# Performance work log

Hardware: AMD Instinct MI355X
Metric: run time of the kernel (lower is better)

Reference implementation:

```python
import jax, jax.numpy as jnp
import numpy as np

B, N, DIN, D, H, L, DOUT = 32, 512, 256, 256, 8, 2, 256
DH = D // H
EPS = 1e-5
MAX_DEG, NUM_SPATIAL = 1000, 100


def _bn(x, g, b):
    # torch BatchNorm1d training-mode normalization (biased variance over dim 0)
    m = x.mean(0)
    v = x.var(0)
    return (x - m) * jax.lax.rsqrt(v + EPS) * g + b


def _ln(x, g, b):
    m = x.mean(-1, keepdims=True)
    v = x.var(-1, keepdims=True)
    return (x - m) * jax.lax.rsqrt(v + EPS) * g + b


def _leaky(x):
    return jnp.where(x >= 0, x, 0.01 * x)


def setup_inputs() -> dict:
    key = jax.random.key(0)
    ks = iter(jax.random.split(key, 40))
    nrm = lambda shape: jax.random.normal(next(ks), shape, jnp.float32) * 0.02
    inp = {
        "x": jax.random.normal(next(ks), (B * N, DIN), jnp.float32),
        "adj_fc": jax.random.randint(next(ks), (B, N, N), 0, 2, jnp.int32),
        "spd_dist": jax.random.randint(next(ks), (B, N, N), -1, NUM_SPATIAL, jnp.int32),
        # lin_first: Linear + BatchNorm1d + LeakyReLU
        "W_first": nrm((D, DIN)), "b_first": jnp.zeros((D,), jnp.float32),
        "bn1_g": jnp.ones((D,), jnp.float32), "bn1_b": jnp.zeros((D,), jnp.float32),
        # embeddings (spd_embedding has padding_idx=0 -> zero row)
        "deg_emb": nrm((MAX_DEG, D)),
        "spd_emb": nrm((NUM_SPATIAL, H)).at[0].set(0.0),
        # stacked TransformerEncoderLayer params [L, ...]
        "Wqkv": nrm((L, 3 * D, D)), "bqkv": jnp.zeros((L, 3 * D), jnp.float32),
        "Wo": nrm((L, D, D)), "bo": jnp.zeros((L, D), jnp.float32),
        "ln1_g": jnp.ones((L, D), jnp.float32), "ln1_b": jnp.zeros((L, D), jnp.float32),
        "W1": nrm((L, D, D)), "b1": jnp.zeros((L, D), jnp.float32),
        "W2": nrm((L, D, D)), "b2": jnp.zeros((L, D), jnp.float32),
        "ln2_g": jnp.ones((L, D), jnp.float32), "ln2_b": jnp.zeros((L, D), jnp.float32),
        # lin_in: Linear + BatchNorm1d + LeakyReLU
        "W_in": nrm((DOUT, D)), "b_in": jnp.zeros((DOUT,), jnp.float32),
        "bn2_g": jnp.ones((DOUT,), jnp.float32), "bn2_b": jnp.zeros((DOUT,), jnp.float32),
    }
    return inp


def _forward(x, adj_fc, spd_dist, W_first, b_first, bn1_g, bn1_b, deg_emb, spd_emb,
             Wqkv, bqkv, Wo, bo, ln1_g, ln1_b, W1, b1, W2, b2, ln2_g, ln2_b,
             W_in, b_in, bn2_g, bn2_b):
    h = _leaky(_bn(x @ W_first.T + b_first, bn1_g, bn1_b)).reshape(B, N, D)
    # degree bias: adj_fc.bool().sum(1) -> [B, N]
    deg = (adj_fc != 0).sum(1)
    h = h + deg_emb[deg]
    # SPD-based per-head additive attention bias
    neg = spd_dist < 0
    am = spd_emb[jnp.where(neg, 0, spd_dist)]            # [B, N, N, H]
    am = jnp.where(neg[..., None], -1.0, am)
    # torch.cat over dim 0 per head -> [H*B, N, N]; torch MHA then consumes it
    # row-major as (b*H + h); replicate that exact (buggy-but-faithful) layout
    bias = jnp.concatenate([am[..., i] for i in range(H)], axis=0).reshape(B, H, N, N)
    scale = 1.0 / np.sqrt(DH).astype(np.float32)
    for l in range(L):
        qkv = h @ Wqkv[l].T + bqkv[l]                    # [B, N, 3D]
        q, k, v = jnp.split(qkv, 3, axis=-1)
        q = q.reshape(B, N, H, DH).transpose(0, 2, 1, 3)
        k = k.reshape(B, N, H, DH).transpose(0, 2, 1, 3)
        v = v.reshape(B, N, H, DH).transpose(0, 2, 1, 3)
        s = jnp.einsum('bhqd,bhkd->bhqk', q, k) * scale + bias
        p = jax.nn.softmax(s, axis=-1)
        o = jnp.einsum('bhqk,bhkd->bhqd', p, v).transpose(0, 2, 1, 3).reshape(B, N, D)
        h = _ln(h + o @ Wo[l].T + bo[l], ln1_g[l], ln1_b[l])  # post-norm
        f = jax.nn.relu(h @ W1[l].T + b1[l]) @ W2[l].T + b2[l]
        h = _ln(h + f, ln2_g[l], ln2_b[l])
    return _leaky(_bn(h.reshape(B * N, D) @ W_in.T + b_in, bn2_g, bn2_b))


def reference(x, adj_fc, spd_dist, W_first, b_first, bn1_g, bn1_b, deg_emb, spd_emb,
              Wqkv, bqkv, Wo, bo, ln1_g, ln1_b, W1, b1, W2, b2, ln2_g, ln2_b,
              W_in, b_in, bn2_g, bn2_b):
    return _forward(x, adj_fc, spd_dist, W_first, b_first, bn1_g, bn1_b, deg_emb,
                    spd_emb, Wqkv, bqkv, Wo, bo, ln1_g, ln1_b, W1, b1, W2, b2,
                    ln2_g, ln2_b, W_in, b_in, bn2_g, bn2_b)
```

## Files before the change

### kernel.cpp

```cpp
#include <hip/hip_runtime.h>
#include <hip/hip_bf16.h>
#include <math.h>

#define B_   32
#define N_   512
#define D_   256
#define H_   8
#define DH_  32
#define L_   2
#define ROWS (B_ * N_)
#define EPS_ 1e-5f

typedef __attribute__((ext_vector_type(8))) short bf16x8;
typedef __attribute__((ext_vector_type(4))) float f32x4;

__device__ __forceinline__ short f2bf(float f) {
    unsigned u = __builtin_bit_cast(unsigned, f);
    u += 0x7fffu + ((u >> 16) & 1u);
    return (short)(u >> 16);
}

__device__ __forceinline__ void gl_lds16(const short* g, short* l) {
    __builtin_amdgcn_global_load_lds(
        (const __attribute__((address_space(1))) unsigned int*)g,
        (__attribute__((address_space(3))) unsigned int*)l, 16, 0, 0);
}

__global__ __launch_bounds__(256) void cvt_all(const float* __restrict__ x,
                                               const float* __restrict__ wf,
                                               const float* __restrict__ wq,
                                               const float* __restrict__ wo,
                                               const float* __restrict__ w1,
                                               const float* __restrict__ w2,
                                               const float* __restrict__ wi,
                                               short* __restrict__ xb,
                                               short* __restrict__ wb)
{
    const int u = blockIdx.x * 256 + threadIdx.x;
    if (u >= 638976) return;
    const float* s; short* d; int off;
    if      (u < 524288) { s = x;  d = xb;          off = u; }
    else if (u < 532480) { s = wf; d = wb;          off = u - 524288; }
    else if (u < 581632) { s = wq; d = wb + 65536;  off = u - 532480; }
    else if (u < 598016) { s = wo; d = wb + 458752; off = u - 581632; }
    else if (u < 614400) { s = w1; d = wb + 589824; off = u - 598016; }
    else if (u < 630784) { s = w2; d = wb + 720896; off = u - 614400; }
    else                 { s = wi; d = wb + 851968; off = u - 630784; }
    const float4 a = ((const float4*)s)[off * 2];
    const float4 b = ((const float4*)s)[off * 2 + 1];
    bf16x8 o;
    o[0] = f2bf(a.x); o[1] = f2bf(a.y); o[2] = f2bf(a.z); o[3] = f2bf(a.w);
    o[4] = f2bf(b.x); o[5] = f2bf(b.y); o[6] = f2bf(b.z); o[7] = f2bf(b.w);
    *(bf16x8*)(d + (size_t)off * 8) = o;
}

#define GSTAGE(buf, kb)                                                        \
    {                                                                          \
        _Pragma("unroll")                                                      \
        for (int j = 0; j < 4; j++) {                                          \
            const int ra = srow + j * 8;                                       \
            const int sw = (sslot ^ (ra & 7)) << 3;                            \
            gl_lds16(A  + (size_t)(m0 + ra) * K + (kb) + sw,                   \
                     &Al[buf][(w * 32 + j * 8) * 64]);                         \
            gl_lds16(Bw + (size_t)(n0 + ra) * K + (kb) + sw,                   \
                     &Bl[buf][(w * 32 + j * 8) * 64]);                         \
        }                                                                      \
    }

template<int FLAGS>
__global__ __launch_bounds__(256) void gemm_bf16(const short* __restrict__ A,
                                                 const short* __restrict__ Bw,
                                                 const float* __restrict__ bias,
                                                 float* __restrict__ Cf,
                                                 short* __restrict__ Cb,
                                                 int M, int Nn, int K)
{
    __shared__ short Al[2][128 * 64];
    __shared__ short Bl[2][128 * 64];
    const int t = threadIdx.x, w = t >> 6, l = t & 63;
    const int lg = l >> 4, lr = l & 15;
    const int wm = w >> 1, wn = w & 1;
    const int m0 = blockIdx.x * 128, n0 = blockIdx.y * 128;
    const int srow = w * 32 + (l >> 3), sslot = l & 7;

    f32x4 acc[4][4] = {};

    GSTAGE(0, 0);
    __syncthreads();
    int cur = 0;
    for (int kb = 64; kb < K + 64; kb += 64) {
        if (kb < K) GSTAGE(cur ^ 1, kb);
        #pragma unroll
        for (int ks = 0; ks < 2; ks++) {
            bf16x8 af[4], bfr[4];
            #pragma unroll
            for (int i = 0; i < 4; i++) {
                const int ar = wm * 64 + i * 16 + lr;
                af[i]  = *(const bf16x8*)&Al[cur][ar * 64 + (((lg + ks * 4) ^ (ar & 7)) << 3)];
                const int br = wn * 64 + i * 16 + lr;
                bfr[i] = *(const bf16x8*)&Bl[cur][br * 64 + (((lg + ks * 4) ^ (br & 7)) << 3)];
            }
            #pragma unroll
            for (int mi = 0; mi < 4; mi++)
                #pragma unroll
                for (int ni = 0; ni < 4; ni++)
                    acc[mi][ni] = __builtin_amdgcn_mfma_f32_16x16x32_bf16(af[mi], bfr[ni],
                                                                          acc[mi][ni], 0, 0, 0);
        }
        __syncthreads();
        cur ^= 1;
    }

    #pragma unroll
    for (int ni = 0; ni < 4; ni++) {
        const int n = n0 + wn * 64 + ni * 16 + lr;
        const float bv = bias[n];
        const float qs = ((FLAGS & 8) && n < 256) ? 0.17677669529663687f : 1.0f;
        #pragma unroll
        for (int mi = 0; mi < 4; mi++) {
            #pragma unroll
            for (int r = 0; r < 4; r++) {
                const int m = m0 + wm * 64 + mi * 16 + 4 * lg + r;
                float v = (acc[mi][ni][r] + bv) * qs;
                if (FLAGS & 4) v = fmaxf(v, 0.f);
                if (FLAGS & 1) Cf[(size_t)m * Nn + n] = v;
                if (FLAGS & 2) Cb[(size_t)m * Nn + n] = f2bf(v);
            }
        }
    }
}

__global__ __launch_bounds__(256) void bn_partial(const float* __restrict__ Y,
                                                  float* __restrict__ part)
{
    const int t = threadIdx.x, blk = blockIdx.x;
    float s = 0.f, sq = 0.f;
    const float* p = Y + (size_t)blk * 256 * 256 + t;
    for (int r = 0; r < 256; r++) {
        float v = p[(size_t)r * 256];
        s += v; sq += v * v;
    }
    part[t * 64 + blk]         = s;
    part[16384 + t * 64 + blk] = sq;
}

__global__ __launch_bounds__(256) void bn_finalize(const float* __restrict__ part,
                                                   const float* __restrict__ g,
                                                   const float* __restrict__ b,
                                                   float* __restrict__ sc)
{
    const int t = threadIdx.x;
    float s = 0.f, sq = 0.f;
    #pragma unroll
    for (int i = 0; i < 16; i++) {
        const float4 a = *(const float4*)&part[t * 64 + i * 4];
        const float4 q = *(const float4*)&part[16384 + t * 64 + i * 4];
        s  += (a.x + a.y) + (a.z + a.w);
        sq += (q.x + q.y) + (q.z + q.w);
    }
    const float mean = s * (1.f / (float)ROWS);
    const float var  = sq * (1.f / (float)ROWS) - mean * mean;
    const float k    = g[t] * rsqrtf(var + EPS_);
    sc[t]       = k;
    sc[256 + t] = b[t] - mean * k;
}

__global__ __launch_bounds__(256) void bn_apply_leaky(const float* __restrict__ Y,
                                                      const float* __restrict__ sc,
                                                      float* __restrict__ O)
{
    const int idx = blockIdx.x * 256 + threadIdx.x;
    const int c4  = (idx & 63) * 4;
    const float4 v  = *(const float4*)&Y[(size_t)idx * 4];
    const float4 k  = *(const float4*)&sc[c4];
    const float4 sh = *(const float4*)&sc[256 + c4];
    float4 o;
    o.x = fmaf(v.x, k.x, sh.x); o.x = o.x >= 0.f ? o.x : 0.01f * o.x;
    o.y = fmaf(v.y, k.y, sh.y); o.y = o.y >= 0.f ? o.y : 0.01f * o.y;
    o.z = fmaf(v.z, k.z, sh.z); o.z = o.z >= 0.f ? o.z : 0.01f * o.z;
    o.w = fmaf(v.w, k.w, sh.w); o.w = o.w >= 0.f ? o.w : 0.01f * o.w;
    *(float4*)&O[(size_t)idx * 4] = o;
}

__global__ __launch_bounds__(256) void bn_deg(const float* __restrict__ Y,
                                              const float* __restrict__ sc,
                                              const int* __restrict__ deg,
                                              const float* __restrict__ emb,
                                              float* __restrict__ h,
                                              short* __restrict__ hb)
{
    const int idx = blockIdx.x * 256 + threadIdx.x;
    const int row = idx >> 6;
    const int c4  = (idx & 63) * 4;
    const float4 v  = *(const float4*)&Y[(size_t)idx * 4];
    const float4 k  = *(const float4*)&sc[c4];
    const float4 sh = *(const float4*)&sc[256 + c4];
    const int d = deg[row];
    const float4 e = *(const float4*)&emb[(size_t)d * 256 + c4];
    float4 o;
    o.x = fmaf(v.x, k.x, sh.x); o.x = (o.x >= 0.f ? o.x : 0.01f * o.x) + e.x;
    o.y = fmaf(v.y, k.y, sh.y); o.y = (o.y >= 0.f ? o.y : 0.01f * o.y) + e.y;
    o.z = fmaf(v.z, k.z, sh.z); o.z = (o.z >= 0.f ? o.z : 0.01f * o.z) + e.z;
    o.w = fmaf(v.w, k.w, sh.w); o.w = (o.w >= 0.f ? o.w : 0.01f * o.w) + e.w;
    *(float4*)&h[(size_t)idx * 4] = o;
    short4 s4; s4.x = f2bf(o.x); s4.y = f2bf(o.y); s4.z = f2bf(o.z); s4.w = f2bf(o.w);
    *(short4*)&hb[(size_t)idx * 4] = s4;
}

__global__ __launch_bounds__(256) void deg_kernel(const int* __restrict__ adj,
                                                  int* __restrict__ deg)
{
    __shared__ int sm[4][64];
    const int b = blockIdx.x, j0 = blockIdx.y * 64;
    const int tg = threadIdx.x >> 6, lane = threadIdx.x & 63;
    const int* p = adj + (size_t)b * N_ * N_ + j0 + lane;
    int c = 0;
    #pragma unroll 4
    for (int i = tg; i < N_; i += 4) c += (p[(size_t)i * N_] != 0);
    sm[tg][lane] = c;
    __syncthreads();
    if (threadIdx.x < 64)
        deg[b * N_ + j0 + threadIdx.x] =
            sm[0][threadIdx.x] + sm[1][threadIdx.x] + sm[2][threadIdx.x] + sm[3][threadIdx.x];
}

__global__ __launch_bounds__(256) void add_ln2(float* __restrict__ h,
                                               short* __restrict__ hb,
                                               const float* __restrict__ p,
                                               const float* __restrict__ g,
                                               const float* __restrict__ be)
{
    const int wv = threadIdx.x >> 6, ln = threadIdx.x & 63;
    const size_t row  = (size_t)blockIdx.x * 4 + wv;
    const size_t base = row * 256 + ln * 4;
    const float4 a = *(const float4*)&h[base];
    const float4 q = *(const float4*)&p[base];
    const float v0 = a.x + q.x, v1 = a.y + q.y, v2 = a.z + q.z, v3 = a.w + q.w;
    float s  = v0 + v1 + v2 + v3;
    float sq = v0 * v0 + v1 * v1 + v2 * v2 + v3 * v3;
    #pragma unroll
    for (int m = 1; m < 64; m <<= 1) {
        s  += __shfl_xor(s,  m, 64);
        sq += __shfl_xor(sq, m, 64);
    }
    const float mean = s * (1.f / 256.f);
    const float var  = sq * (1.f / 256.f) - mean * mean;
    const float r    = rsqrtf(var + EPS_);
    const float4 gg = *(const float4*)&g[ln * 4];
    const float4 bb = *(const float4*)&be[ln * 4];
    float4 o;
    o.x = (v0 - mean) * r * gg.x + bb.x;
    o.y = (v1 - mean) * r * gg.y + bb.y;
    o.z = (v2 - mean) * r * gg.z + bb.z;
    o.w = (v3 - mean) * r * gg.w + bb.w;
    *(float4*)&h[base] = o;
    short4 sb; sb.x = f2bf(o.x); sb.y = f2bf(o.y); sb.z = f2bf(o.z); sb.w = f2bf(o.w);
    *(short4*)&hb[base] = sb;
}

#define KST 40
#define VST 136
#define PST 136

__global__ __launch_bounds__(256) void attn_mfma(const short* __restrict__ qkv,
                                                 const int* __restrict__ spd,
                                                 const float* __restrict__ semb,
                                                 short* __restrict__ out)
{
    __shared__ short Kl[128 * KST];
    __shared__ short Vl[32 * VST + 64];
    __shared__ short Pl[4][16 * PST];
    __shared__ float sembL[128];

    const int t  = threadIdx.x, w = t >> 6, l = t & 63;
    const int lg = l >> 4, lr = l & 15;

    const int s   = ((blockIdx.x & 7) << 7) + (blockIdx.x >> 3);
    const int bs  = s >> 5, ie = (s >> 2) & 7, qb = s & 3;
    const int b   = (ie * 32 + bs) >> 3, hd = (ie * 32 + bs) & 7;
    const int q0  = qb * 128 + w * 32;

    if (t < 100) sembL[t] = semb[t * 8 + ie];

    bf16x8 qf[2];
    #pragma unroll
    for (int qt = 0; qt < 2; qt++)
        qf[qt] = *(const bf16x8*)&qkv[((size_t)b * N_ + q0 + qt * 16 + lr) * 768 + hd * 32 + lg * 8];

    f32x4 oacc[2][2] = {};
    float mrun[2] = {-INFINITY, -INFINITY}, srun[2] = {0.f, 0.f};

    const int sr = t >> 1, shf = (t & 1) << 4;
    const int vofs = (t & 1) * 32;
    const short* kgBase = qkv + ((size_t)b * N_ + sr) * 768 + 256 + hd * 32 + shf;

    bf16x8 nk0 = *(const bf16x8*)(kgBase);
    bf16x8 nk1 = *(const bf16x8*)(kgBase + 8);
    bf16x8 nv0 = *(const bf16x8*)(kgBase + 256);
    bf16x8 nv1 = *(const bf16x8*)(kgBase + 264);
    *(bf16x8*)&Kl[sr * KST + shf]     = nk0;
    *(bf16x8*)&Kl[sr * KST + shf + 8] = nk1;
    #pragma unroll
    for (int i = 0; i < 8; i++) {
        Vl[(shf + i)     * VST + vofs + sr] = nv0[i];
        Vl[(shf + 8 + i) * VST + vofs + sr] = nv1[i];
    }
    __syncthreads();

    for (int ti = 0; ti < 4; ti++) {
        const int k0 = ti * 128;
        bf16x8 kfr[8];
        #pragma unroll
        for (int ct = 0; ct < 8; ct++)
            kfr[ct] = *(const bf16x8*)&Kl[(ct * 16 + lr) * KST + lg * 8];
        bf16x8 vfr[4][2];
        #pragma unroll
        for (int kt = 0; kt < 4; kt++)
            #pragma unroll
            for (int c2 = 0; c2 < 2; c2++)
                vfr[kt][c2] = *(const bf16x8*)&Vl[(c2 * 16 + lr) * VST + c2 * 32 + kt * 32 + lg * 8];

        const short* kgN = kgBase + (size_t)(((ti + 1) & 3) * 128) * 768;
        nk0 = *(const bf16x8*)(kgN);
        nk1 = *(const bf16x8*)(kgN + 8);
        nv0 = *(const bf16x8*)(kgN + 256);
        nv1 = *(const bf16x8*)(kgN + 264);

        #pragma unroll
        for (int qt = 0; qt < 2; qt++) {
            const int4* sp4 = (const int4*)(spd + ((size_t)bs * N_ + q0 + qt * 16 + lr) * N_ + k0);
            f32x4 sA[8];
            #pragma unroll
            for (int ct = 0; ct < 8; ct++) {
                const int4 sv = sp4[ct * 4 + lg];
                f32x4 c;
                c[0] = (sv.x < 0) ? -1.0f : sembL[sv.x];
                c[1] = (sv.y < 0) ? -1.0f : sembL[sv.y];
                c[2] = (sv.z < 0) ? -1.0f : sembL[sv.z];
                c[3] = (sv.w < 0) ? -1.0f : sembL[sv.w];
                sA[ct] = c;
            }
            #pragma unroll
            for (int ct = 0; ct < 8; ct++)
                sA[ct] = __builtin_amdgcn_mfma_f32_16x16x32_bf16(kfr[ct], qf[qt], sA[ct], 0, 0, 0);

            float m = sA[0][0];
            #pragma unroll
            for (int ct = 0; ct < 8; ct++)
                #pragma unroll
                for (int r = 0; r < 4; r++) m = fmaxf(m, sA[ct][r]);
            m = fmaxf(m, __shfl_xor(m, 16, 64));
            m = fmaxf(m, __shfl_xor(m, 32, 64));
            const float mnew  = fmaxf(mrun[qt], m);
            const float alpha = __expf(mrun[qt] - mnew);
            mrun[qt] = mnew;

            float ps = 0.f;
            #pragma unroll
            for (int ct = 0; ct < 8; ct++) {
                float p0 = __expf(sA[ct][0] - mnew);
                float p1 = __expf(sA[ct][1] - mnew);
                float p2 = __expf(sA[ct][2] - mnew);
                float p3 = __expf(sA[ct][3] - mnew);
                ps += (p0 + p1) + (p2 + p3);
                short4 pk; pk.x = f2bf(p0); pk.y = f2bf(p1); pk.z = f2bf(p2); pk.w = f2bf(p3);
                *(short4*)&Pl[w][lr * PST + ct * 16 + 4 * lg] = pk;
            }
            ps += __shfl_xor(ps, 16, 64);
            ps += __shfl_xor(ps, 32, 64);
            srun[qt] = srun[qt] * alpha + ps;
            oacc[qt][0] *= alpha;
            oacc[qt][1] *= alpha;

            #pragma unroll
            for (int kt = 0; kt < 4; kt++) {
                const bf16x8 pa = *(const bf16x8*)&Pl[w][lr * PST + kt * 32 + lg * 8];
                #pragma unroll
                for (int c2 = 0; c2 < 2; c2++)
                    oacc[qt][c2] = __builtin_amdgcn_mfma_f32_16x16x32_bf16(vfr[kt][c2], pa,
                                                                           oacc[qt][c2], 0, 0, 0);
            }
        }

        if (ti < 3) {
            __syncthreads();
            *(bf16x8*)&Kl[sr * KST + shf]     = nk0;
            *(bf16x8*)&Kl[sr * KST + shf + 8] = nk1;
            #pragma unroll
            for (int i = 0; i < 8; i++) {
                Vl[(shf + i)     * VST + vofs + sr] = nv0[i];
                Vl[(shf + 8 + i) * VST + vofs + sr] = nv1[i];
            }
            __syncthreads();
        }
    }

    #pragma unroll
    for (int qt = 0; qt < 2; qt++) {
        const float inv = 1.f / srun[qt];
        #pragma unroll
        for (int c2 = 0; c2 < 2; c2++) {
            short4 s4;
            s4.x = f2bf(oacc[qt][c2][0] * inv);
            s4.y = f2bf(oacc[qt][c2][1] * inv);
            s4.z = f2bf(oacc[qt][c2][2] * inv);
            s4.w = f2bf(oacc[qt][c2][3] * inv);
            *(short4*)&out[((size_t)b * N_ + q0 + qt * 16 + lr) * 256 + hd * 32 + c2 * 16 + 4 * lg] = s4;
        }
    }
}

extern "C" void kernel_launch(void* const* d_in, const int* in_sizes, int n_in,
                              void* d_out, int out_size, void* d_ws, size_t ws_size,
                              hipStream_t stream)
{
    const float* x    = (const float*)d_in[0];
    const int*   adj  = (const int*)  d_in[1];
    const int*   spd  = (const int*)  d_in[2];
    const float* Wf   = (const float*)d_in[3];
    const float* bf   = (const float*)d_in[4];
    const float* bn1g = (const float*)d_in[5];
    const float* bn1b = (const float*)d_in[6];
    const float* degE = (const float*)d_in[7];
    const float* semb = (const float*)d_in[8];
    const float* Wqkv = (const float*)d_in[9];
    const float* bqkv = (const float*)d_in[10];
    const float* Wo   = (const float*)d_in[11];
    const float* bo   = (const float*)d_in[12];
    const float* ln1g = (const float*)d_in[13];
    const float* ln1b = (const float*)d_in[14];
    const float* W1   = (const float*)d_in[15];
    const float* b1   = (const float*)d_in[16];
    const float* W2   = (const float*)d_in[17];
    const float* b2   = (const float*)d_in[18];
    const float* ln2g = (const float*)d_in[19];
    const float* ln2b = (const float*)d_in[20];
    const float* Win  = (const float*)d_in[21];
    const float* bin  = (const float*)d_in[22];
    const float* bn2g = (const float*)d_in[23];
    const float* bn2b = (const float*)d_in[24];

    char* p = (char*)d_ws;
    float* h    = (float*)p;  p += (size_t)ROWS * 256 * 4;
    float* t3   = (float*)p;  p += (size_t)ROWS * 256 * 4;
    char*  shr  = p;          p += (size_t)ROWS * 768 * 2;
    float* t1   = (float*)shr;
    short* qkvb = (short*)shr;
    short* hb   = (short*)p;  p += (size_t)ROWS * 256 * 2;
    short* t2b  = (short*)p;  p += (size_t)ROWS * 256 * 2;
    short* xb   = (short*)p;  p += (size_t)ROWS * 256 * 2;
    short* wb   = (short*)p;  p += (size_t)917504 * 2;
    int*   deg  = (int*)p;    p += (size_t)ROWS * 4;
    float* bnp  = (float*)p;  p += 64 * 512 * 4;
    float* bnf  = (float*)p;

    const short* wfb = wb;
    const short* wqb = wb + 65536;
    const short* wob = wb + 458752;
    const short* w1b = wb + 589824;
    const short* w2b = wb + 720896;
    const short* wib = wb + 851968;

    const dim3 blk(256);
    const dim3 g256(128, 2);
    const dim3 g768(128, 6);

    cvt_all<<<2496, blk, 0, stream>>>(x, Wf, Wqkv, Wo, W1, W2, Win, xb, wb);
    deg_kernel<<<dim3(B_, 8), blk, 0, stream>>>(adj, deg);

    gemm_bf16<1><<<g256, blk, 0, stream>>>(xb, wfb, bf, t1, nullptr, ROWS, 256, 256);
    bn_partial <<<64, blk, 0, stream>>>(t1, bnp);
    bn_finalize<<<1,  blk, 0, stream>>>(bnp, bn1g, bn1b, bnf);
    bn_deg<<<ROWS * 256 / 4 / 256, blk, 0, stream>>>(t1, bnf, deg, degE, h, hb);

    for (int l = 0; l < L_; l++) {
        gemm_bf16<2 | 8><<<g768, blk, 0, stream>>>(hb, wqb + (size_t)l * 768 * 256,
                                                   bqkv + l * 768, nullptr, qkvb, ROWS, 768, 256);
        attn_mfma<<<1024, blk, 0, stream>>>(qkvb, spd, semb, t2b);
        gemm_bf16<1><<<g256, blk, 0, stream>>>(t2b, wob + (size_t)l * 256 * 256,
                                               bo + l * 256, t3, nullptr, ROWS, 256, 256);
        add_ln2<<<ROWS / 4, blk, 0, stream>>>(h, hb, t3, ln1g + l * 256, ln1b + l * 256);
        gemm_bf16<2 | 4><<<g256, blk, 0, stream>>>(hb, w1b + (size_t)l * 256 * 256,
                                                   b1 + l * 256, nullptr, t2b, ROWS, 256, 256);
        gemm_bf16<1><<<g256, blk, 0, stream>>>(t2b, w2b + (size_t)l * 256 * 256,
                                               b2 + l * 256, t3, nullptr, ROWS, 256, 256);
        add_ln2<<<ROWS / 4, blk, 0, stream>>>(h, hb, t3, ln2g + l * 256, ln2b + l * 256);
    }

    gemm_bf16<1><<<g256, blk, 0, stream>>>(hb, wib, bin, t1, nullptr, ROWS, 256, 256);
    bn_partial <<<64, blk, 0, stream>>>(t1, bnp);
    bn_finalize<<<1,  blk, 0, stream>>>(bnp, bn2g, bn2b, bnf);
    bn_apply_leaky<<<ROWS * 256 / 4 / 256, blk, 0, stream>>>(t1, bnf, (float*)d_out);
}
```

Before: 493.5 us.

## Shrink GEMM tiles to 64x64, restructure attention score path and bf16 packing

The GEMM tile drops from 128x128 to 64x64 and the grids grow to match. This raises the number of blocks and the occupancy on the many-CU GPU, at the cost of less data reuse per tile. In attention, the spd bias loads are issued earlier and the QK MFMAs start from a zero accumulator, with the bias added afterwards so load latency can overlap compute. The max and sum reductions become trees, and the manual bf16 rounding is replaced with the hardware v_cvt_pk_bf16_f32 instruction.

Measured after the change: 488.9 us. Within noise of the previous version (-0.9%).

```diff
diff --git a/kernel.cpp b/kernel.cpp
--- a/kernel.cpp
+++ b/kernel.cpp
@@ -18,6 +18,12 @@
     unsigned u = __builtin_bit_cast(unsigned, f);
     u += 0x7fffu + ((u >> 16) & 1u);
     return (short)(u >> 16);
+}
+
+__device__ __forceinline__ unsigned cvtpk(float lo, float hi) {
+    unsigned r;
+    asm("v_cvt_pk_bf16_f32 %0, %1, %2" : "=v"(r) : "v"(lo), "v"(hi));
+    return r;
 }
 
 __device__ __forceinline__ void gl_lds16(const short* g, short* l) {
@@ -54,17 +60,18 @@
     *(bf16x8*)(d + (size_t)off * 8) = o;
 }
 
-#define GSTAGE(buf, kb)                                                        \
-    {                                                                          \
-        _Pragma("unroll")                                                      \
-        for (int j = 0; j < 4; j++) {                                          \
-            const int ra = srow + j * 8;                                       \
-            const int sw = (sslot ^ (ra & 7)) << 3;                            \
-            gl_lds16(A  + (size_t)(m0 + ra) * K + (kb) + sw,                   \
-                     &Al[buf][(w * 32 + j * 8) * 64]);                         \
-            gl_lds16(Bw + (size_t)(n0 + ra) * K + (kb) + sw,                   \
-                     &Bl[buf][(w * 32 + j * 8) * 64]);                         \
-        }                                                                      \
+#define GSTAGE64(buf, kb)                                                    \
+    {                                                                        \
+        _Pragma("unroll")                                                    \
+        for (int j = 0; j < 2; j++) {                                        \
+            const int slot = w * 128 + j * 64 + l;                           \
+            const int row = slot >> 3, c = slot & 7;                         \
+            const int sw = (c ^ (row & 7)) << 3;                             \
+            gl_lds16(A  + (size_t)(m0 + row) * K + (kb) + sw,                \
+                     &Al[buf][(w * 128 + j * 64) * 8]);                      \
+            gl_lds16(Bw + (size_t)(n0 + row) * K + (kb) + sw,                \
+                     &Bl[buf][(w * 128 + j * 64) * 8]);                      \
+        }                                                                    \
     }
 
 template<int FLAGS>
@@ -75,35 +82,34 @@
                                                  short* __restrict__ Cb,
                                                  int M, int Nn, int K)
 {
-    __shared__ short Al[2][128 * 64];
-    __shared__ short Bl[2][128 * 64];
+    __shared__ short Al[2][64 * 64];
+    __shared__ short Bl[2][64 * 64];
     const int t = threadIdx.x, w = t >> 6, l = t & 63;
     const int lg = l >> 4, lr = l & 15;
     const int wm = w >> 1, wn = w & 1;
-    const int m0 = blockIdx.x * 128, n0 = blockIdx.y * 128;
-    const int srow = w * 32 + (l >> 3), sslot = l & 7;
-
-    f32x4 acc[4][4] = {};
-
-    GSTAGE(0, 0);
+    const int m0 = blockIdx.x * 64, n0 = blockIdx.y * 64;
+
+    f32x4 acc[2][2] = {};
+
+    GSTAGE64(0, 0);
     __syncthreads();
     int cur = 0;
     for (int kb = 64; kb < K + 64; kb += 64) {
-        if (kb < K) GSTAGE(cur ^ 1, kb);
+        if (kb < K) GSTAGE64(cur ^ 1, kb);
         #pragma unroll
         for (int ks = 0; ks < 2; ks++) {
-            bf16x8 af[4], bfr[4];
-            #pragma unroll
-            for (int i = 0; i < 4; i++) {
-                const int ar = wm * 64 + i * 16 + lr;
+            bf16x8 af[2], bfr[2];
+            #pragma unroll
+            for (int i = 0; i < 2; i++) {
+                const int ar = wm * 32 + i * 16 + lr;
                 af[i]  = *(const bf16x8*)&Al[cur][ar * 64 + (((lg + ks * 4) ^ (ar & 7)) << 3)];
-                const int br = wn * 64 + i * 16 + lr;
+                const int br = wn * 32 + i * 16 + lr;
                 bfr[i] = *(const bf16x8*)&Bl[cur][br * 64 + (((lg + ks * 4) ^ (br & 7)) << 3)];
             }
             #pragma unroll
-            for (int mi = 0; mi < 4; mi++)
+            for (int mi = 0; mi < 2; mi++)
                 #pragma unroll
-                for (int ni = 0; ni < 4; ni++)
+                for (int ni = 0; ni < 2; ni++)
                     acc[mi][ni] = __builtin_amdgcn_mfma_f32_16x16x32_bf16(af[mi], bfr[ni],
                                                                           acc[mi][ni], 0, 0, 0);
         }
@@ -112,15 +118,15 @@
     }
 
     #pragma unroll
-    for (int ni = 0; ni < 4; ni++) {
-        const int n = n0 + wn * 64 + ni * 16 + lr;
+    for (int ni = 0; ni < 2; ni++) {
+        const int n = n0 + wn * 32 + ni * 16 + lr;
         const float bv = bias[n];
         const float qs = ((FLAGS & 8) && n < 256) ? 0.17677669529663687f : 1.0f;
         #pragma unroll
-        for (int mi = 0; mi < 4; mi++) {
+        for (int mi = 0; mi < 2; mi++) {
             #pragma unroll
             for (int r = 0; r < 4; r++) {
-                const int m = m0 + wm * 64 + mi * 16 + 4 * lg + r;
+                const int m = m0 + wm * 32 + mi * 16 + 4 * lg + r;
                 float v = (acc[mi][ni][r] + bv) * qs;
                 if (FLAGS & 4) v = fmaxf(v, 0.f);
                 if (FLAGS & 1) Cf[(size_t)m * Nn + n] = v;
@@ -307,65 +313,86 @@
     }
     __syncthreads();
 
+    const f32x4 zc = {0.f, 0.f, 0.f, 0.f};
+
     for (int ti = 0; ti < 4; ti++) {
         const int k0 = ti * 128;
+
+        int4 sv0[8];
+        {
+            const int4* sp0 = (const int4*)(spd + ((size_t)bs * N_ + q0 + lr) * N_ + k0);
+            #pragma unroll
+            for (int ct = 0; ct < 8; ct++) sv0[ct] = sp0[ct * 4 + lg];
+        }
+
         bf16x8 kfr[8];
         #pragma unroll
         for (int ct = 0; ct < 8; ct++)
             kfr[ct] = *(const bf16x8*)&Kl[(ct * 16 + lr) * KST + lg * 8];
-        bf16x8 vfr[4][2];
-        #pragma unroll
-        for (int kt = 0; kt < 4; kt++)
-            #pragma unroll
-            for (int c2 = 0; c2 < 2; c2++)
-                vfr[kt][c2] = *(const bf16x8*)&Vl[(c2 * 16 + lr) * VST + c2 * 32 + kt * 32 + lg * 8];
-
+
+        f32x4 sA[8];
+        #pragma unroll
+        for (int ct = 0; ct < 8; ct++)
+            sA[ct] = __builtin_amdgcn_mfma_f32_16x16x32_bf16(kfr[ct], qf[0], zc, 0, 0, 0);
+
+        int4 sv1[8];
+        {
+            const int4* sp1 = (const int4*)(spd + ((size_t)bs * N_ + q0 + 16 + lr) * N_ + k0);
+            #pragma unroll
+            for (int ct = 0; ct < 8; ct++) sv1[ct] = sp1[ct * 4 + lg];
+        }
         const short* kgN = kgBase + (size_t)(((ti + 1) & 3) * 128) * 768;
         nk0 = *(const bf16x8*)(kgN);
         nk1 = *(const bf16x8*)(kgN + 8);
         nv0 = *(const bf16x8*)(kgN + 256);
         nv1 = *(const bf16x8*)(kgN + 264);
+        bf16x8 vfr[4][2];
+        #pragma unroll
+        for (int kt = 0; kt < 4; kt++)
+            #pragma unroll
+            for (int c2 = 0; c2 < 2; c2++)
+                vfr[kt][c2] = *(const bf16x8*)&Vl[(c2 * 16 + lr) * VST + c2 * 32 + kt * 32 + lg * 8];
 
         #pragma unroll
         for (int qt = 0; qt < 2; qt++) {
-            const int4* sp4 = (const int4*)(spd + ((size_t)bs * N_ + q0 + qt * 16 + lr) * N_ + k0);
-            f32x4 sA[8];
+            if (qt == 1) {
+                #pragma unroll
+                for (int ct = 0; ct < 8; ct++)
+                    sA[ct] = __builtin_amdgcn_mfma_f32_16x16x32_bf16(kfr[ct], qf[1], zc, 0, 0, 0);
+            }
             #pragma unroll
             for (int ct = 0; ct < 8; ct++) {
-                const int4 sv = sp4[ct * 4 + lg];
-                f32x4 c;
-                c[0] = (sv.x < 0) ? -1.0f : sembL[sv.x];
-                c[1] = (sv.y < 0) ? -1.0f : sembL[sv.y];
-                c[2] = (sv.z < 0) ? -1.0f : sembL[sv.z];
-                c[3] = (sv.w < 0) ? -1.0f : sembL[sv.w];
-                sA[ct] = c;
-            }
+                const int4 sv = (qt == 0) ? sv0[ct] : sv1[ct];
+                sA[ct][0] += (sv.x < 0) ? -1.0f : sembL[sv.x];
+                sA[ct][1] += (sv.y < 0) ? -1.0f : sembL[sv.y];
+                sA[ct][2] += (sv.z < 0) ? -1.0f : sembL[sv.z];
+                sA[ct][3] += (sv.w < 0) ? -1.0f : sembL[sv.w];
+            }
+            float mx[8];
             #pragma unroll
             for (int ct = 0; ct < 8; ct++)
-                sA[ct] = __builtin_amdgcn_mfma_f32_16x16x32_bf16(kfr[ct], qf[qt], sA[ct], 0, 0, 0);
-
-            float m = sA[0][0];
-            #pragma unroll
-            for (int ct = 0; ct < 8; ct++)
-                #pragma unroll
-                for (int r = 0; r < 4; r++) m = fmaxf(m, sA[ct][r]);
+                mx[ct] = fmaxf(fmaxf(sA[ct][0], sA[ct][1]), fmaxf(sA[ct][2], sA[ct][3]));
+            float m = fmaxf(fmaxf(fmaxf(mx[0], mx[1]), fmaxf(mx[2], mx[3])),
+                            fmaxf(fmaxf(mx[4], mx[5]), fmaxf(mx[6], mx[7])));
             m = fmaxf(m, __shfl_xor(m, 16, 64));
             m = fmaxf(m, __shfl_xor(m, 32, 64));
             const float mnew  = fmaxf(mrun[qt], m);
             const float alpha = __expf(mrun[qt] - mnew);
             mrun[qt] = mnew;
 
-            float ps = 0.f;
+            float ps4[8];
             #pragma unroll
             for (int ct = 0; ct < 8; ct++) {
-                float p0 = __expf(sA[ct][0] - mnew);
-                float p1 = __expf(sA[ct][1] - mnew);
-                float p2 = __expf(sA[ct][2] - mnew);
-                float p3 = __expf(sA[ct][3] - mnew);
-                ps += (p0 + p1) + (p2 + p3);
-                short4 pk; pk.x = f2bf(p0); pk.y = f2bf(p1); pk.z = f2bf(p2); pk.w = f2bf(p3);
-                *(short4*)&Pl[w][lr * PST + ct * 16 + 4 * lg] = pk;
-            }
+                const float e0 = __expf(sA[ct][0] - mnew);
+                const float e1 = __expf(sA[ct][1] - mnew);
+                const float e2 = __expf(sA[ct][2] - mnew);
+                const float e3 = __expf(sA[ct][3] - mnew);
+                ps4[ct] = (e0 + e1) + (e2 + e3);
+                uint2 pk; pk.x = cvtpk(e0, e1); pk.y = cvtpk(e2, e3);
+                *(uint2*)&Pl[w][lr * PST + ct * 16 + 4 * lg] = pk;
+            }
+            float ps = (((ps4[0] + ps4[1]) + (ps4[2] + ps4[3])) +
+                        ((ps4[4] + ps4[5]) + (ps4[6] + ps4[7])));
             ps += __shfl_xor(ps, 16, 64);
             ps += __shfl_xor(ps, 32, 64);
             srun[qt] = srun[qt] * alpha + ps;
@@ -400,12 +427,10 @@
         const float inv = 1.f / srun[qt];
         #pragma unroll
         for (int c2 = 0; c2 < 2; c2++) {
-            short4 s4;
-            s4.x = f2bf(oacc[qt][c2][0] * inv);
-            s4.y = f2bf(oacc[qt][c2][1] * inv);
-            s4.z = f2bf(oacc[qt][c2][2] * inv);
-            s4.w = f2bf(oacc[qt][c2][3] * inv);
-            *(short4*)&out[((size_t)b * N_ + q0 + qt * 16 + lr) * 256 + hd * 32 + c2 * 16 + 4 * lg] = s4;
+            uint2 o2;
+            o2.x = cvtpk(oacc[qt][c2][0] * inv, oacc[qt][c2][1] * inv);
+            o2.y = cvtpk(oacc[qt][c2][2] * inv, oacc[qt][c2][3] * inv);
+            *(uint2*)&out[((size_t)b * N_ + q0 + qt * 16 + lr) * 256 + hd * 32 + c2 * 16 + 4 * lg] = o2;
         }
     }
 }
@@ -462,8 +487,8 @@
     const short* wib = wb + 851968;
 
     const dim3 blk(256);
-    const dim3 g256(128, 2);
-    const dim3 g768(128, 6);
+    const dim3 g256(ROWS / 64, 4);
+    const dim3 g768(ROWS / 64, 12);
 
     cvt_all<<<2496, blk, 0, stream>>>(x, Wf, Wqkv, Wo, W1, W2, Win, xb, wb);
     deg_kernel<<<dim3(B_, 8), blk, 0, stream>>>(adj, deg);
```
